# Optimization experiments

Measured on AMD Instinct MI355X. Metric: run time of the kernel, lower is better.

The kernel has to match this reference:

```python
import jax, jax.numpy as jnp
import numpy as np

B, N, D_IN = 256, 64, 128   # batch, n_agents, input_dim
H0, H1, H2 = 256, 256, 64   # rnn_hidden_dim[0], [1], [2]


def setup_inputs() -> dict:
    key = jax.random.key(0)
    ks = jax.random.split(key, 14)
    s = 0.05
    return {
        "obs": jax.random.normal(ks[0], (B, N, D_IN), dtype=jnp.float32),
        "W_enc": jax.random.normal(ks[1], (H0, D_IN), dtype=jnp.float32) * s,
        "b_enc": jax.random.normal(ks[2], (H0,), dtype=jnp.float32) * s,
        "W_obs": jax.random.normal(ks[3], (H0, H0), dtype=jnp.float32) * s,
        "b_obs": jax.random.normal(ks[4], (H0,), dtype=jnp.float32) * s,
        "W_ih": jax.random.normal(ks[5], (3 * H0, H0), dtype=jnp.float32) * s,
        "b_ih": jax.random.normal(ks[6], (3 * H0,), dtype=jnp.float32) * s,
        "W_hh": jax.random.normal(ks[7], (3 * H0, H0), dtype=jnp.float32) * s,
        "b_hh": jax.random.normal(ks[8], (3 * H0,), dtype=jnp.float32) * s,
        "W_val": jax.random.normal(ks[9], (H1, H0), dtype=jnp.float32) * s,
        "b_val": jax.random.normal(ks[10], (H1,), dtype=jnp.float32) * s,
        "W_dec": jax.random.normal(ks[11], (H2, H1), dtype=jnp.float32) * s,
        "b_dec": jax.random.normal(ks[12], (H2,), dtype=jnp.float32) * s,
    }


def reference(obs, W_enc, b_enc, W_obs, b_obs, W_ih, b_ih, W_hh, b_hh,
              W_val, b_val, W_dec, b_dec):
    # encoding + f_obs  -> h: [B, N, H0]
    x = jax.nn.relu(jnp.einsum("bnd,hd->bnh", obs, W_enc) + b_enc)
    h = jnp.einsum("bnh,gh->bng", x, W_obs) + b_obs

    # comm: mean over other agents. Original masks self and divides by N
    # (mean over dim of size N with self zeroed) => (sum_all - self) / N.
    c = (jnp.sum(h, axis=1, keepdims=True) - h) / N  # [B, N, H0]

    # GRUCell(input=c, hidden=h), PyTorch gate ordering r, z, n
    gi = jnp.einsum("bnh,gh->bng", c, W_ih) + b_ih   # [B, N, 3*H0]
    gh = jnp.einsum("bnh,gh->bng", h, W_hh) + b_hh
    gi_r, gi_z, gi_n = jnp.split(gi, 3, axis=-1)
    gh_r, gh_z, gh_n = jnp.split(gh, 3, axis=-1)
    r = jax.nn.sigmoid(gi_r + gh_r)
    z = jax.nn.sigmoid(gi_z + gh_z)
    n = jnp.tanh(gi_n + r * gh_n)
    h = (1.0 - z) * n + z * h  # [B, N, H0]

    # value head + decoding; seq_len=1 squeezed -> [B, N, H2]
    v = jnp.einsum("bnh,vh->bnv", h, W_val) + b_val
    out = jnp.einsum("bnv,ov->bno", v, W_dec) + b_dec
    return out
```

## Files before the change

kernel.cpp:

```cpp
#include <hip/hip_runtime.h>
#include <hip/hip_bf16.h>
#include <math.h>


typedef __bf16  bf16x8 __attribute__((ext_vector_type(8)));
typedef float   f32x4  __attribute__((ext_vector_type(4)));

#define DIN 128
#define H0  256
#define SW  264
#define SWO 136
#define LOG2E 1.44269504088896f

#define O_WENC 0
#define O_WOBS 32768
#define O_WIH  98304
#define O_WHH  294912
#define O_WVAL 491520
#define O_WDEC 557056
#define W_TOT  573440

__device__ __forceinline__ f32x4 mfma16(bf16x8 a, bf16x8 b, f32x4 c) {
    return __builtin_amdgcn_mfma_f32_16x16x32_bf16(a, b, c, 0, 0, 0);
}
__device__ __forceinline__ float bf2f(__hip_bfloat16 x) { return __bfloat162float(x); }
__device__ __forceinline__ __hip_bfloat16 f2bf(float x) { return __float2bfloat16(x); }

__device__ __forceinline__ float fsigmoid(float x) {
    float e = __builtin_amdgcn_exp2f(-LOG2E * x);
    return __builtin_amdgcn_rcpf(1.0f + e);
}
__device__ __forceinline__ float ftanh(float x) {
    float e = __builtin_amdgcn_exp2f(2.0f * LOG2E * x);
    return 1.0f - 2.0f * __builtin_amdgcn_rcpf(1.0f + e);
}

__device__ __forceinline__ bf16x8 w8(const __hip_bfloat16* p, int idx) {
    return *(const bf16x8*)(p + idx);
}

__device__ __forceinline__ int tadr(int r, int k) { return r * SW + k; }
__device__ __forceinline__ int oadr(int r, int k) { return r * SWO + k; }

__global__ __launch_bounds__(256) void prep_kernel(
    const float* __restrict__ W_enc, const float* __restrict__ W_obs,
    const float* __restrict__ W_ih,  const float* __restrict__ W_hh,
    const float* __restrict__ W_val, const float* __restrict__ W_dec,
    __hip_bfloat16* __restrict__ ws)
{
    const int i = (blockIdx.x * 256 + threadIdx.x) * 8;
    if (i >= W_TOT) return;
    const float* src; int off;
    if      (i < O_WOBS) { src = W_enc; off = O_WENC; }
    else if (i < O_WIH)  { src = W_obs; off = O_WOBS; }
    else if (i < O_WHH)  { src = W_ih;  off = O_WIH;  }
    else if (i < O_WVAL) { src = W_hh;  off = O_WHH;  }
    else if (i < O_WDEC) { src = W_val; off = O_WVAL; }
    else                 { src = W_dec; off = O_WDEC; }
    const float* f = src + (i - off);
    f32x4 a = *(const f32x4*)f;
    f32x4 b = *(const f32x4*)(f + 4);
    bf16x8 v;
    #pragma unroll
    for (int j = 0; j < 4; j++) { v[j] = (__bf16)a[j]; v[j + 4] = (__bf16)b[j]; }
    *(bf16x8*)(ws + i) = v;
}

__global__ __launch_bounds__(512, 2) void commnet_mfma(
    const __hip_bfloat16* __restrict__ ws,
    const float* __restrict__ b_enc, const float* __restrict__ b_obs,
    const float* __restrict__ b_ih,  const float* __restrict__ b_hh,
    const float* __restrict__ b_val, const float* __restrict__ b_dec,
    const float* __restrict__ obs,   float* __restrict__ out)
{
    __shared__ __align__(16) __hip_bfloat16 T0[64 * SW];
    __shared__ __align__(16) __hip_bfloat16 T1[64 * SW];

    const __hip_bfloat16* W_enc = ws + O_WENC;
    const __hip_bfloat16* W_obs = ws + O_WOBS;
    const __hip_bfloat16* W_ih  = ws + O_WIH;
    const __hip_bfloat16* W_hh  = ws + O_WHH;
    const __hip_bfloat16* W_val = ws + O_WVAL;
    const __hip_bfloat16* W_dec = ws + O_WDEC;

    const int tid  = threadIdx.x;
    const int wave = tid >> 6;
    const int lane = tid & 63;
    const int quad = lane >> 4;
    const int lc   = lane & 15;
    const int row0 = blockIdx.x * 64;
    const int ko16 = quad * 8;

    for (int i = tid; i < 64 * DIN / 8; i += 512) {
        const int r = i >> 4;
        const int c = (i & 15) << 3;
        const float* src = obs + (row0 + r) * DIN + c;
        f32x4 a = *(const f32x4*)src;
        f32x4 b = *(const f32x4*)(src + 4);
        bf16x8 v;
        #pragma unroll
        for (int j = 0; j < 4; j++) { v[j] = (__bf16)a[j]; v[j + 4] = (__bf16)b[j]; }
        *(bf16x8*)&T1[oadr(r, c)] = v;
    }
    __syncthreads();

    #pragma unroll
    for (int cp = 0; cp < 2; cp++) {
        const int n = (wave + 8 * cp) * 16 + lc;
        const float bias = b_enc[n];
        f32x4 acc[4] = {};
        #pragma unroll
        for (int k0 = 0; k0 < DIN; k0 += 32) {
            const int kk = k0 + ko16;
            bf16x8 b = w8(W_enc, n * DIN + kk);
            #pragma unroll
            for (int rt = 0; rt < 4; rt++) {
                bf16x8 a = *(const bf16x8*)&T1[oadr(rt * 16 + lc, kk)];
                acc[rt] = mfma16(a, b, acc[rt]);
            }
        }
        #pragma unroll
        for (int rt = 0; rt < 4; rt++)
            #pragma unroll
            for (int i = 0; i < 4; i++) {
                const int row = rt * 16 + quad * 4 + i;
                T0[tadr(row, n)] = f2bf(fmaxf(acc[rt][i] + bias, 0.0f));
            }
    }
    __syncthreads();

    #pragma unroll
    for (int cp = 0; cp < 2; cp++) {
        const int n = (wave + 8 * cp) * 16 + lc;
        const float bias = b_obs[n];
        f32x4 acc[4] = {};
        #pragma unroll 2
        for (int k0 = 0; k0 < H0; k0 += 32) {
            const int kk = k0 + ko16;
            bf16x8 b = w8(W_obs, n * H0 + kk);
            #pragma unroll
            for (int rt = 0; rt < 4; rt++) {
                bf16x8 a = *(const bf16x8*)&T0[tadr(rt * 16 + lc, kk)];
                acc[rt] = mfma16(a, b, acc[rt]);
            }
        }
        #pragma unroll
        for (int rt = 0; rt < 4; rt++)
            #pragma unroll
            for (int i = 0; i < 4; i++) {
                const int row = rt * 16 + quad * 4 + i;
                T1[tadr(row, n)] = f2bf(acc[rt][i] + bias);
            }
    }
    __syncthreads();

    #pragma unroll
    for (int cp = 0; cp < 2; cp++) {
        const int n = (wave + 8 * cp) * 16 + lc;
        const float bir = b_ih[n], biz = b_ih[n + 256], bin = b_ih[n + 512];
        const float bhr = b_hh[n], bhz = b_hh[n + 256], bhn = b_hh[n + 512];
        f32x4 gir[4] = {}, giz[4] = {}, gin[4] = {};
        f32x4 ghr[4] = {}, ghz[4] = {}, ghn[4] = {};
        #pragma unroll 2
        for (int k0 = 0; k0 < H0; k0 += 32) {
            const int kk = k0 + ko16;
            bf16x8 bir8 = w8(W_ih, (n      ) * H0 + kk);
            bf16x8 biz8 = w8(W_ih, (n + 256) * H0 + kk);
            bf16x8 bin8 = w8(W_ih, (n + 512) * H0 + kk);
            bf16x8 bhr8 = w8(W_hh, (n      ) * H0 + kk);
            bf16x8 bhz8 = w8(W_hh, (n + 256) * H0 + kk);
            bf16x8 bhn8 = w8(W_hh, (n + 512) * H0 + kk);
            #pragma unroll
            for (int rt = 0; rt < 4; rt++) {
                bf16x8 aH = *(const bf16x8*)&T1[tadr(rt * 16 + lc, kk)];
                gir[rt] = mfma16(aH, bir8, gir[rt]);
                giz[rt] = mfma16(aH, biz8, giz[rt]);
                gin[rt] = mfma16(aH, bin8, gin[rt]);
                ghr[rt] = mfma16(aH, bhr8, ghr[rt]);
                ghz[rt] = mfma16(aH, bhz8, ghz[rt]);
                ghn[rt] = mfma16(aH, bhn8, ghn[rt]);
            }
        }
        float Sr = 0.0f, Sz = 0.0f, Sn = 0.0f;
        #pragma unroll
        for (int rt = 0; rt < 4; rt++)
            #pragma unroll
            for (int i = 0; i < 4; i++) {
                Sr += gir[rt][i]; Sz += giz[rt][i]; Sn += gin[rt][i];
            }
        Sr += __shfl_xor(Sr, 16); Sr += __shfl_xor(Sr, 32);
        Sz += __shfl_xor(Sz, 16); Sz += __shfl_xor(Sz, 32);
        Sn += __shfl_xor(Sn, 16); Sn += __shfl_xor(Sn, 32);

        #pragma unroll
        for (int rt = 0; rt < 4; rt++)
            #pragma unroll
            for (int i = 0; i < 4; i++) {
                const int row = rt * 16 + quad * 4 + i;
                const float gi_r = (Sr - gir[rt][i]) * (1.0f / 64.0f) + bir;
                const float gi_z = (Sz - giz[rt][i]) * (1.0f / 64.0f) + biz;
                const float gi_n = (Sn - gin[rt][i]) * (1.0f / 64.0f) + bin;
                const float r  = fsigmoid(gi_r + ghr[rt][i] + bhr);
                const float z  = fsigmoid(gi_z + ghz[rt][i] + bhz);
                const float nn = ftanh(gi_n + r * (ghn[rt][i] + bhn));
                const float h  = bf2f(T1[tadr(row, n)]);
                T0[tadr(row, n)] = f2bf((1.0f - z) * nn + z * h);
            }
    }
    __syncthreads();

    #pragma unroll
    for (int cp = 0; cp < 2; cp++) {
        const int n = (wave + 8 * cp) * 16 + lc;
        const float bias = b_val[n];
        f32x4 acc[4] = {};
        #pragma unroll 2
        for (int k0 = 0; k0 < H0; k0 += 32) {
            const int kk = k0 + ko16;
            bf16x8 b = w8(W_val, n * H0 + kk);
            #pragma unroll
            for (int rt = 0; rt < 4; rt++) {
                bf16x8 a = *(const bf16x8*)&T0[tadr(rt * 16 + lc, kk)];
                acc[rt] = mfma16(a, b, acc[rt]);
            }
        }
        #pragma unroll
        for (int rt = 0; rt < 4; rt++)
            #pragma unroll
            for (int i = 0; i < 4; i++) {
                const int row = rt * 16 + quad * 4 + i;
                T1[tadr(row, n)] = f2bf(acc[rt][i] + bias);
            }
    }
    __syncthreads();

    {
        const int ct  = wave & 3;
        const int rtb = (wave >> 2) * 2;
        const int n   = ct * 16 + lc;
        const float bias = b_dec[n];
        f32x4 acc[2] = {};
        #pragma unroll 2
        for (int k0 = 0; k0 < H0; k0 += 32) {
            const int kk = k0 + ko16;
            bf16x8 b = w8(W_dec, n * H0 + kk);
            #pragma unroll
            for (int j = 0; j < 2; j++) {
                bf16x8 a = *(const bf16x8*)&T1[tadr((rtb + j) * 16 + lc, kk)];
                acc[j] = mfma16(a, b, acc[j]);
            }
        }
        #pragma unroll
        for (int j = 0; j < 2; j++)
            #pragma unroll
            for (int i = 0; i < 4; i++) {
                const int row = (rtb + j) * 16 + quad * 4 + i;
                out[(row0 + row) * 64 + n] = acc[j][i] + bias;
            }
    }
}

extern "C" void kernel_launch(void* const* d_in, const int* in_sizes, int n_in,
                              void* d_out, int out_size, void* d_ws, size_t ws_size,
                              hipStream_t stream) {
    (void)in_sizes; (void)n_in; (void)out_size; (void)ws_size;
    const float* obs   = (const float*)d_in[0];
    const float* W_enc = (const float*)d_in[1];  const float* b_enc = (const float*)d_in[2];
    const float* W_obs = (const float*)d_in[3];  const float* b_obs = (const float*)d_in[4];
    const float* W_ih  = (const float*)d_in[5];  const float* b_ih  = (const float*)d_in[6];
    const float* W_hh  = (const float*)d_in[7];  const float* b_hh  = (const float*)d_in[8];
    const float* W_val = (const float*)d_in[9];  const float* b_val = (const float*)d_in[10];
    const float* W_dec = (const float*)d_in[11]; const float* b_dec = (const float*)d_in[12];
    float* out = (float*)d_out;
    __hip_bfloat16* ws = (__hip_bfloat16*)d_ws;

    prep_kernel<<<280, 256, 0, stream>>>(W_enc, W_obs, W_ih, W_hh, W_val, W_dec, ws);
    commnet_mfma<<<256, 512, 0, stream>>>(
        ws, b_enc, b_obs, b_ih, b_hh, b_val, b_dec, obs, out);
}
```

Measured before the change: 122.6 us.

## Split fused kernel into encoder and GRU kernels with 32-row blocks

Splits the single fused kernel into two launches: an encoder kernel that writes h to workspace along with per-block column sums, and a GRU/value/decode kernel that reads them back. Each block now handles 32 rows, so there are 512 blocks instead of 256, which gives more blocks per CU. The communication term is computed as an MFMA of the column sum against W_ih, so the per-row input-gate matmuls are no longer scaled. Costs include an extra launch, a global round trip of h, and the gi matmul still running on h; a fallback to the fused kernel is kept for when the workspace is too small.

```diff
diff --git a/kernel.cpp b/kernel.cpp
--- a/kernel.cpp
+++ b/kernel.cpp
@@ -19,6 +19,9 @@
 #define O_WVAL 491520
 #define O_WDEC 557056
 #define W_TOT  573440
+#define O_H    573440
+#define B_PARTS 9535488
+#define WS_NEED (9535488 + 524288)
 
 __device__ __forceinline__ f32x4 mfma16(bf16x8 a, bf16x8 b, f32x4 c) {
     return __builtin_amdgcn_mfma_f32_16x16x32_bf16(a, b, c, 0, 0, 0);
@@ -34,13 +37,9 @@
     float e = __builtin_amdgcn_exp2f(2.0f * LOG2E * x);
     return 1.0f - 2.0f * __builtin_amdgcn_rcpf(1.0f + e);
 }
-
 __device__ __forceinline__ bf16x8 w8(const __hip_bfloat16* p, int idx) {
     return *(const bf16x8*)(p + idx);
 }
-
-__device__ __forceinline__ int tadr(int r, int k) { return r * SW + k; }
-__device__ __forceinline__ int oadr(int r, int k) { return r * SWO + k; }
 
 __global__ __launch_bounds__(256) void prep_kernel(
     const float* __restrict__ W_enc, const float* __restrict__ W_obs,
@@ -66,7 +65,229 @@
     *(bf16x8*)(ws + i) = v;
 }
 
-__global__ __launch_bounds__(512, 2) void commnet_mfma(
+__global__ __launch_bounds__(512, 2) void k_enc(
+    const __hip_bfloat16* __restrict__ ws,
+    const float* __restrict__ b_enc, const float* __restrict__ b_obs,
+    const float* __restrict__ obs,
+    __hip_bfloat16* __restrict__ Hws, float* __restrict__ parts)
+{
+    __shared__ __align__(16) __hip_bfloat16 OB[32 * SWO];
+    __shared__ __align__(16) __hip_bfloat16 X1[32 * SW];
+    __shared__ __align__(16) __hip_bfloat16 HT[32 * SW];
+
+    const __hip_bfloat16* W_enc = ws + O_WENC;
+    const __hip_bfloat16* W_obs = ws + O_WOBS;
+
+    const int tid  = threadIdx.x;
+    const int wave = tid >> 6;
+    const int lane = tid & 63;
+    const int quad = lane >> 4;
+    const int lc   = lane & 15;
+    const int ko16 = quad * 8;
+    const int R0   = blockIdx.x * 32;
+
+    {
+        const int r = tid >> 4;
+        const int c = (tid & 15) << 3;
+        const float* src = obs + (R0 + r) * DIN + c;
+        f32x4 a = *(const f32x4*)src;
+        f32x4 b = *(const f32x4*)(src + 4);
+        bf16x8 v;
+        #pragma unroll
+        for (int j = 0; j < 4; j++) { v[j] = (__bf16)a[j]; v[j + 4] = (__bf16)b[j]; }
+        *(bf16x8*)&OB[r * SWO + c] = v;
+    }
+    __syncthreads();
+
+    #pragma unroll
+    for (int cp = 0; cp < 2; cp++) {
+        const int n = (wave + 8 * cp) * 16 + lc;
+        const float bias = b_enc[n];
+        f32x4 acc[2] = {};
+        #pragma unroll
+        for (int k0 = 0; k0 < DIN; k0 += 32) {
+            const int kk = k0 + ko16;
+            bf16x8 b = w8(W_enc, n * DIN + kk);
+            #pragma unroll
+            for (int rt = 0; rt < 2; rt++) {
+                bf16x8 a = *(const bf16x8*)&OB[(rt * 16 + lc) * SWO + kk];
+                acc[rt] = mfma16(a, b, acc[rt]);
+            }
+        }
+        #pragma unroll
+        for (int rt = 0; rt < 2; rt++)
+            #pragma unroll
+            for (int i = 0; i < 4; i++)
+                X1[(rt * 16 + quad * 4 + i) * SW + n] = f2bf(fmaxf(acc[rt][i] + bias, 0.0f));
+    }
+    __syncthreads();
+
+    #pragma unroll
+    for (int cp = 0; cp < 2; cp++) {
+        const int n = (wave + 8 * cp) * 16 + lc;
+        const float bias = b_obs[n];
+        f32x4 acc[2] = {};
+        #pragma unroll 2
+        for (int k0 = 0; k0 < H0; k0 += 32) {
+            const int kk = k0 + ko16;
+            bf16x8 b = w8(W_obs, n * H0 + kk);
+            #pragma unroll
+            for (int rt = 0; rt < 2; rt++) {
+                bf16x8 a = *(const bf16x8*)&X1[(rt * 16 + lc) * SW + kk];
+                acc[rt] = mfma16(a, b, acc[rt]);
+            }
+        }
+        float colp = 0.0f;
+        #pragma unroll
+        for (int rt = 0; rt < 2; rt++)
+            #pragma unroll
+            for (int i = 0; i < 4; i++) {
+                const float v = acc[rt][i] + bias;
+                HT[(rt * 16 + quad * 4 + i) * SW + n] = f2bf(v);
+                colp += v;
+            }
+        colp += __shfl_xor(colp, 16);
+        colp += __shfl_xor(colp, 32);
+        if (quad == 0) parts[blockIdx.x * 256 + n] = colp;
+    }
+    __syncthreads();
+
+    {
+        const int r = tid >> 4;
+        const int c = (tid << 4) & 255;
+        *(bf16x8*)&Hws[(R0 + r) * 256 + c]     = *(const bf16x8*)&HT[r * SW + c];
+        *(bf16x8*)&Hws[(R0 + r) * 256 + c + 8] = *(const bf16x8*)&HT[r * SW + c + 8];
+    }
+}
+
+__global__ __launch_bounds__(512, 2) void k_gru(
+    const __hip_bfloat16* __restrict__ ws,
+    const float* __restrict__ b_ih,  const float* __restrict__ b_hh,
+    const float* __restrict__ b_val, const float* __restrict__ b_dec,
+    const __hip_bfloat16* __restrict__ Hws, const float* __restrict__ parts,
+    float* __restrict__ out)
+{
+    __shared__ __align__(16) __hip_bfloat16 HT[32 * SW];
+    __shared__ __align__(16) __hip_bfloat16 HP[32 * SW];
+    __shared__ __align__(16) __hip_bfloat16 CS[256];
+
+    const __hip_bfloat16* W_ih  = ws + O_WIH;
+    const __hip_bfloat16* W_hh  = ws + O_WHH;
+    const __hip_bfloat16* W_val = ws + O_WVAL;
+    const __hip_bfloat16* W_dec = ws + O_WDEC;
+
+    const int tid  = threadIdx.x;
+    const int wave = tid >> 6;
+    const int lane = tid & 63;
+    const int quad = lane >> 4;
+    const int lc   = lane & 15;
+    const int ko16 = quad * 8;
+    const int R0   = blockIdx.x * 32;
+    const int pb   = blockIdx.x & ~1;
+
+    {
+        const int r = tid >> 4;
+        const int c = (tid << 4) & 255;
+        *(bf16x8*)&HT[r * SW + c]     = *(const bf16x8*)&Hws[(R0 + r) * 256 + c];
+        *(bf16x8*)&HT[r * SW + c + 8] = *(const bf16x8*)&Hws[(R0 + r) * 256 + c + 8];
+        if (tid < 256)
+            CS[tid] = f2bf(parts[pb * 256 + tid] + parts[(pb + 1) * 256 + tid]);
+    }
+    __syncthreads();
+
+    #pragma unroll
+    for (int cp = 0; cp < 2; cp++) {
+        const int n = (wave + 8 * cp) * 16 + lc;
+        const float bir = b_ih[n], biz = b_ih[n + 256], bin = b_ih[n + 512];
+        const float bhr = b_hh[n], bhz = b_hh[n + 256], bhn = b_hh[n + 512];
+        f32x4 gir[2] = {}, giz[2] = {}, gin[2] = {};
+        f32x4 ghr[2] = {}, ghz[2] = {}, ghn[2] = {};
+        f32x4 sr = {}, sz = {}, sn = {};
+        #pragma unroll 2
+        for (int k0 = 0; k0 < H0; k0 += 32) {
+            const int kk = k0 + ko16;
+            bf16x8 csA = *(const bf16x8*)&CS[kk];
+            bf16x8 bir8 = w8(W_ih, (n      ) * H0 + kk);
+            bf16x8 biz8 = w8(W_ih, (n + 256) * H0 + kk);
+            bf16x8 bin8 = w8(W_ih, (n + 512) * H0 + kk);
+            bf16x8 bhr8 = w8(W_hh, (n      ) * H0 + kk);
+            bf16x8 bhz8 = w8(W_hh, (n + 256) * H0 + kk);
+            bf16x8 bhn8 = w8(W_hh, (n + 512) * H0 + kk);
+            sr = mfma16(csA, bir8, sr);
+            sz = mfma16(csA, biz8, sz);
+            sn = mfma16(csA, bin8, sn);
+            #pragma unroll
+            for (int rt = 0; rt < 2; rt++) {
+                bf16x8 aH = *(const bf16x8*)&HT[(rt * 16 + lc) * SW + kk];
+                gir[rt] = mfma16(aH, bir8, gir[rt]);
+                giz[rt] = mfma16(aH, biz8, giz[rt]);
+                gin[rt] = mfma16(aH, bin8, gin[rt]);
+                ghr[rt] = mfma16(aH, bhr8, ghr[rt]);
+                ghz[rt] = mfma16(aH, bhz8, ghz[rt]);
+                ghn[rt] = mfma16(aH, bhn8, ghn[rt]);
+            }
+        }
+        const float s_r = sr[0], s_z = sz[0], s_n = sn[0];
+        #pragma unroll
+        for (int rt = 0; rt < 2; rt++)
+            #pragma unroll
+            for (int i = 0; i < 4; i++) {
+                const int row = rt * 16 + quad * 4 + i;
+                const float gi_r = (s_r - gir[rt][i]) * (1.0f / 64.0f) + bir;
+                const float gi_z = (s_z - giz[rt][i]) * (1.0f / 64.0f) + biz;
+                const float gi_n = (s_n - gin[rt][i]) * (1.0f / 64.0f) + bin;
+                const float r  = fsigmoid(gi_r + ghr[rt][i] + bhr);
+                const float z  = fsigmoid(gi_z + ghz[rt][i] + bhz);
+                const float nn = ftanh(gi_n + r * (ghn[rt][i] + bhn));
+                const float h  = bf2f(HT[row * SW + n]);
+                HP[row * SW + n] = f2bf((1.0f - z) * nn + z * h);
+            }
+    }
+    __syncthreads();
+
+    #pragma unroll
+    for (int cp = 0; cp < 2; cp++) {
+        const int n = (wave + 8 * cp) * 16 + lc;
+        const float bias = b_val[n];
+        f32x4 acc[2] = {};
+        #pragma unroll 2
+        for (int k0 = 0; k0 < H0; k0 += 32) {
+            const int kk = k0 + ko16;
+            bf16x8 b = w8(W_val, n * H0 + kk);
+            #pragma unroll
+            for (int rt = 0; rt < 2; rt++) {
+                bf16x8 a = *(const bf16x8*)&HP[(rt * 16 + lc) * SW + kk];
+                acc[rt] = mfma16(a, b, acc[rt]);
+            }
+        }
+        #pragma unroll
+        for (int rt = 0; rt < 2; rt++)
+            #pragma unroll
+            for (int i = 0; i < 4; i++)
+                HT[(rt * 16 + quad * 4 + i) * SW + n] = f2bf(acc[rt][i] + bias);
+    }
+    __syncthreads();
+
+    {
+        const int ct = wave & 3;
+        const int rt = wave >> 2;
+        const int n  = ct * 16 + lc;
+        const float bias = b_dec[n];
+        f32x4 acc = {};
+        #pragma unroll 2
+        for (int k0 = 0; k0 < H0; k0 += 32) {
+            const int kk = k0 + ko16;
+            bf16x8 b = w8(W_dec, n * H0 + kk);
+            bf16x8 a = *(const bf16x8*)&HT[(rt * 16 + lc) * SW + kk];
+            acc = mfma16(a, b, acc);
+        }
+        #pragma unroll
+        for (int i = 0; i < 4; i++)
+            out[(R0 + rt * 16 + quad * 4 + i) * 64 + n] = acc[i] + bias;
+    }
+}
+
+__global__ __launch_bounds__(512, 2) void commnet_fused(
     const __hip_bfloat16* __restrict__ ws,
     const float* __restrict__ b_enc, const float* __restrict__ b_obs,
     const float* __restrict__ b_ih,  const float* __restrict__ b_hh,
@@ -100,7 +321,7 @@
         bf16x8 v;
         #pragma unroll
         for (int j = 0; j < 4; j++) { v[j] = (__bf16)a[j]; v[j + 4] = (__bf16)b[j]; }
-        *(bf16x8*)&T1[oadr(r, c)] = v;
+        *(bf16x8*)&T1[r * SWO + c] = v;
     }
     __syncthreads();
 
@@ -115,17 +336,15 @@
             bf16x8 b = w8(W_enc, n * DIN + kk);
             #pragma unroll
             for (int rt = 0; rt < 4; rt++) {
-                bf16x8 a = *(const bf16x8*)&T1[oadr(rt * 16 + lc, kk)];
+                bf16x8 a = *(const bf16x8*)&T1[(rt * 16 + lc) * SWO + kk];
                 acc[rt] = mfma16(a, b, acc[rt]);
             }
         }
         #pragma unroll
         for (int rt = 0; rt < 4; rt++)
             #pragma unroll
-            for (int i = 0; i < 4; i++) {
-                const int row = rt * 16 + quad * 4 + i;
-                T0[tadr(row, n)] = f2bf(fmaxf(acc[rt][i] + bias, 0.0f));
-            }
+            for (int i = 0; i < 4; i++)
+                T0[(rt * 16 + quad * 4 + i) * SW + n] = f2bf(fmaxf(acc[rt][i] + bias, 0.0f));
     }
     __syncthreads();
 
@@ -140,17 +359,15 @@
             bf16x8 b = w8(W_obs, n * H0 + kk);
             #pragma unroll
             for (int rt = 0; rt < 4; rt++) {
-                bf16x8 a = *(const bf16x8*)&T0[tadr(rt * 16 + lc, kk)];
+                bf16x8 a = *(const bf16x8*)&T0[(rt * 16 + lc) * SW + kk];
                 acc[rt] = mfma16(a, b, acc[rt]);
             }
         }
         #pragma unroll
         for (int rt = 0; rt < 4; rt++)
             #pragma unroll
-            for (int i = 0; i < 4; i++) {
-                const int row = rt * 16 + quad * 4 + i;
-                T1[tadr(row, n)] = f2bf(acc[rt][i] + bias);
-            }
+            for (int i = 0; i < 4; i++)
+                T1[(rt * 16 + quad * 4 + i) * SW + n] = f2bf(acc[rt][i] + bias);
     }
     __syncthreads();
 
@@ -172,7 +389,7 @@
             bf16x8 bhn8 = w8(W_hh, (n + 512) * H0 + kk);
             #pragma unroll
             for (int rt = 0; rt < 4; rt++) {
-                bf16x8 aH = *(const bf16x8*)&T1[tadr(rt * 16 + lc, kk)];
+                bf16x8 aH = *(const bf16x8*)&T1[(rt * 16 + lc) * SW + kk];
                 gir[rt] = mfma16(aH, bir8, gir[rt]);
                 giz[rt] = mfma16(aH, biz8, giz[rt]);
                 gin[rt] = mfma16(aH, bin8, gin[rt]);
@@ -191,7 +408,6 @@
         Sr += __shfl_xor(Sr, 16); Sr += __shfl_xor(Sr, 32);
         Sz += __shfl_xor(Sz, 16); Sz += __shfl_xor(Sz, 32);
         Sn += __shfl_xor(Sn, 16); Sn += __shfl_xor(Sn, 32);
-
         #pragma unroll
         for (int rt = 0; rt < 4; rt++)
             #pragma unroll
@@ -203,8 +419,8 @@
                 const float r  = fsigmoid(gi_r + ghr[rt][i] + bhr);
                 const float z  = fsigmoid(gi_z + ghz[rt][i] + bhz);
                 const float nn = ftanh(gi_n + r * (ghn[rt][i] + bhn));
-                const float h  = bf2f(T1[tadr(row, n)]);
-                T0[tadr(row, n)] = f2bf((1.0f - z) * nn + z * h);
+                const float h  = bf2f(T1[row * SW + n]);
+                T0[row * SW + n] = f2bf((1.0f - z) * nn + z * h);
             }
     }
     __syncthreads();
@@ -220,17 +436,15 @@
             bf16x8 b = w8(W_val, n * H0 + kk);
             #pragma unroll
             for (int rt = 0; rt < 4; rt++) {
-                bf16x8 a = *(const bf16x8*)&T0[tadr(rt * 16 + lc, kk)];
+                bf16x8 a = *(const bf16x8*)&T0[(rt * 16 + lc) * SW + kk];
                 acc[rt] = mfma16(a, b, acc[rt]);
             }
         }
         #pragma unroll
         for (int rt = 0; rt < 4; rt++)
             #pragma unroll
-            for (int i = 0; i < 4; i++) {
-                const int row = rt * 16 + quad * 4 + i;
-                T1[tadr(row, n)] = f2bf(acc[rt][i] + bias);
-            }
+            for (int i = 0; i < 4; i++)
+                T1[(rt * 16 + quad * 4 + i) * SW + n] = f2bf(acc[rt][i] + bias);
     }
     __syncthreads();
 
@@ -246,7 +460,7 @@
             bf16x8 b = w8(W_dec, n * H0 + kk);
             #pragma unroll
             for (int j = 0; j < 2; j++) {
-                bf16x8 a = *(const bf16x8*)&T1[tadr((rtb + j) * 16 + lc, kk)];
+                bf16x8 a = *(const bf16x8*)&T1[((rtb + j) * 16 + lc) * SW + kk];
                 acc[j] = mfma16(a, b, acc[j]);
             }
         }
@@ -263,7 +477,7 @@
 extern "C" void kernel_launch(void* const* d_in, const int* in_sizes, int n_in,
                               void* d_out, int out_size, void* d_ws, size_t ws_size,
                               hipStream_t stream) {
-    (void)in_sizes; (void)n_in; (void)out_size; (void)ws_size;
+    (void)in_sizes; (void)n_in; (void)out_size;
     const float* obs   = (const float*)d_in[0];
     const float* W_enc = (const float*)d_in[1];  const float* b_enc = (const float*)d_in[2];
     const float* W_obs = (const float*)d_in[3];  const float* b_obs = (const float*)d_in[4];
@@ -275,6 +489,14 @@
     __hip_bfloat16* ws = (__hip_bfloat16*)d_ws;
 
     prep_kernel<<<280, 256, 0, stream>>>(W_enc, W_obs, W_ih, W_hh, W_val, W_dec, ws);
-    commnet_mfma<<<256, 512, 0, stream>>>(
-        ws, b_enc, b_obs, b_ih, b_hh, b_val, b_dec, obs, out);
-}
+
+    if (ws_size >= (size_t)WS_NEED) {
+        __hip_bfloat16* Hws  = ws + O_H;
+        float* parts = (float*)((char*)d_ws + B_PARTS);
+        k_enc<<<512, 512, 0, stream>>>(ws, b_enc, b_obs, obs, Hws, parts);
+        k_gru<<<512, 512, 0, stream>>>(ws, b_ih, b_hh, b_val, b_dec, Hws, parts, out);
+    } else {
+        commnet_fused<<<256, 512, 0, stream>>>(
+            ws, b_enc, b_obs, b_ih, b_hh, b_val, b_dec, obs, out);
+    }
+}
```

Measured after the change: 160.5 us. +30.9%, slower.

## Stage weights through double-buffered swizzled LDS with cooperative prefetch

Applied to the files above, without the earlier changes.

Weight tiles are now loaded cooperatively by the whole block into a double-buffered LDS buffer. The next 64-wide k-slice is prefetched into registers while MFMAs consume the current one, instead of each lane reading weights straight from global memory. Activation buffers switch from padded strides to an XOR-swizzled layout to avoid bank conflicts. GRU gates are processed one gate at a time across k-blocks. LDS use rises to 128 KB per block, which can cut occupancy below two blocks per CU, and a barrier is added per k-slice.

```diff
diff --git a/kernel.cpp b/kernel.cpp
--- a/kernel.cpp
+++ b/kernel.cpp
@@ -8,8 +8,6 @@
 
 #define DIN 128
 #define H0  256
-#define SW  264
-#define SWO 136
 #define LOG2E 1.44269504088896f
 
 #define O_WENC 0
@@ -25,7 +23,6 @@
 }
 __device__ __forceinline__ float bf2f(__hip_bfloat16 x) { return __bfloat162float(x); }
 __device__ __forceinline__ __hip_bfloat16 f2bf(float x) { return __float2bfloat16(x); }
-
 __device__ __forceinline__ float fsigmoid(float x) {
     float e = __builtin_amdgcn_exp2f(-LOG2E * x);
     return __builtin_amdgcn_rcpf(1.0f + e);
@@ -34,13 +31,60 @@
     float e = __builtin_amdgcn_exp2f(2.0f * LOG2E * x);
     return 1.0f - 2.0f * __builtin_amdgcn_rcpf(1.0f + e);
 }
-
 __device__ __forceinline__ bf16x8 w8(const __hip_bfloat16* p, int idx) {
     return *(const bf16x8*)(p + idx);
 }
 
-__device__ __forceinline__ int tadr(int r, int k) { return r * SW + k; }
-__device__ __forceinline__ int oadr(int r, int k) { return r * SWO + k; }
+__device__ __forceinline__ int tadr(int r, int k) {
+    return (r << 8) + ((((k >> 3) ^ r) & 31) << 3) + (k & 7);
+}
+__device__ __forceinline__ int oadr(int r, int k) {
+    return (r << 7) + ((((k >> 3) ^ r) & 15) << 3) + (k & 7);
+}
+
+struct St4 { bf16x8 v[4]; };
+
+__device__ __forceinline__ St4 ld_sq(const __hip_bfloat16* src, int K, int kb, int tid) {
+    St4 s;
+    #pragma unroll
+    for (int j = 0; j < 4; j++) {
+        const int u = tid + j * 512, n = u >> 3, c = u & 7;
+        s.v[j] = w8(src, n * K + kb * 64 + c * 8);
+    }
+    return s;
+}
+__device__ __forceinline__ void st_sq(__hip_bfloat16* dst, const St4& s, int tid) {
+    #pragma unroll
+    for (int j = 0; j < 4; j++) {
+        const int u = tid + j * 512, n = u >> 3, c = u & 7;
+        *(bf16x8*)&dst[n * 64 + ((c ^ (n & 7)) << 3)] = s.v[j];
+    }
+}
+__device__ __forceinline__ bf16x8 rd_sq(const __hip_bfloat16* wb, int n, int kw) {
+    return *(const bf16x8*)&wb[n * 64 + ((((kw >> 3) ^ (n & 7)) & 7) << 3)];
+}
+
+__device__ __forceinline__ St4 ld_gr(const __hip_bfloat16* Wih, const __hip_bfloat16* Whh,
+                                     int p, int cp, int kb, int tid) {
+    St4 s;
+    #pragma unroll
+    for (int j = 0; j < 4; j++) {
+        const int u = tid + j * 512, g2 = u >> 10, rem = u & 1023, nl = rem >> 3, c = rem & 7;
+        const __hip_bfloat16* m = g2 ? Whh : Wih;
+        s.v[j] = w8(m, (p * 256 + cp * 128 + nl) * 256 + kb * 64 + c * 8);
+    }
+    return s;
+}
+__device__ __forceinline__ void st_gr(__hip_bfloat16* dst, const St4& s, int tid) {
+    #pragma unroll
+    for (int j = 0; j < 4; j++) {
+        const int u = tid + j * 512, g2 = u >> 10, rem = u & 1023, nl = rem >> 3, c = rem & 7;
+        *(bf16x8*)&dst[g2 * 8192 + nl * 64 + ((c ^ (nl & 7)) << 3)] = s.v[j];
+    }
+}
+__device__ __forceinline__ bf16x8 rd_gr(const __hip_bfloat16* wb, int g2, int nl, int kw) {
+    return *(const bf16x8*)&wb[g2 * 8192 + nl * 64 + ((((kw >> 3) ^ (nl & 7)) & 7) << 3)];
+}
 
 __global__ __launch_bounds__(256) void prep_kernel(
     const float* __restrict__ W_enc, const float* __restrict__ W_obs,
@@ -66,15 +110,16 @@
     *(bf16x8*)(ws + i) = v;
 }
 
-__global__ __launch_bounds__(512, 2) void commnet_mfma(
+__global__ __launch_bounds__(512, 2) void commnet_v6(
     const __hip_bfloat16* __restrict__ ws,
     const float* __restrict__ b_enc, const float* __restrict__ b_obs,
     const float* __restrict__ b_ih,  const float* __restrict__ b_hh,
     const float* __restrict__ b_val, const float* __restrict__ b_dec,
     const float* __restrict__ obs,   float* __restrict__ out)
 {
-    __shared__ __align__(16) __hip_bfloat16 T0[64 * SW];
-    __shared__ __align__(16) __hip_bfloat16 T1[64 * SW];
+    __shared__ __align__(16) __hip_bfloat16 T0[16384];
+    __shared__ __align__(16) __hip_bfloat16 T1[16384];
+    __shared__ __align__(16) __hip_bfloat16 WBb[32768];
 
     const __hip_bfloat16* W_enc = ws + O_WENC;
     const __hip_bfloat16* W_obs = ws + O_WOBS;
@@ -90,160 +135,223 @@
     const int lc   = lane & 15;
     const int row0 = blockIdx.x * 64;
     const int ko16 = quad * 8;
-
-    for (int i = tid; i < 64 * DIN / 8; i += 512) {
-        const int r = i >> 4;
-        const int c = (i & 15) << 3;
-        const float* src = obs + (row0 + r) * DIN + c;
-        f32x4 a = *(const f32x4*)src;
-        f32x4 b = *(const f32x4*)(src + 4);
-        bf16x8 v;
-        #pragma unroll
-        for (int j = 0; j < 4; j++) { v[j] = (__bf16)a[j]; v[j + 4] = (__bf16)b[j]; }
-        *(bf16x8*)&T1[oadr(r, c)] = v;
-    }
-    __syncthreads();
-
-    #pragma unroll
-    for (int cp = 0; cp < 2; cp++) {
-        const int n = (wave + 8 * cp) * 16 + lc;
-        const float bias = b_enc[n];
-        f32x4 acc[4] = {};
-        #pragma unroll
-        for (int k0 = 0; k0 < DIN; k0 += 32) {
-            const int kk = k0 + ko16;
-            bf16x8 b = w8(W_enc, n * DIN + kk);
-            #pragma unroll
-            for (int rt = 0; rt < 4; rt++) {
-                bf16x8 a = *(const bf16x8*)&T1[oadr(rt * 16 + lc, kk)];
-                acc[rt] = mfma16(a, b, acc[rt]);
-            }
-        }
-        #pragma unroll
-        for (int rt = 0; rt < 4; rt++)
-            #pragma unroll
-            for (int i = 0; i < 4; i++) {
-                const int row = rt * 16 + quad * 4 + i;
-                T0[tadr(row, n)] = f2bf(fmaxf(acc[rt][i] + bias, 0.0f));
-            }
-    }
-    __syncthreads();
-
-    #pragma unroll
-    for (int cp = 0; cp < 2; cp++) {
-        const int n = (wave + 8 * cp) * 16 + lc;
-        const float bias = b_obs[n];
-        f32x4 acc[4] = {};
-        #pragma unroll 2
+    const int n0   = wave * 16 + lc;
+    const int n1   = n0 + 128;
+
+    {
+        #pragma unroll
+        for (int j = 0; j < 2; j++) {
+            const int u = tid + j * 512;
+            const int r = u >> 4, c = (u & 15) << 3;
+            const float* src = obs + (row0 + r) * DIN + c;
+            f32x4 a = *(const f32x4*)src;
+            f32x4 b = *(const f32x4*)(src + 4);
+            bf16x8 v;
+            #pragma unroll
+            for (int q = 0; q < 4; q++) { v[q] = (__bf16)a[q]; v[q + 4] = (__bf16)b[q]; }
+            *(bf16x8*)&T1[oadr(r, c)] = v;
+        }
+        St4 s0 = ld_sq(W_enc, DIN, 0, tid);
+        st_sq(WBb, s0, tid);
+    }
+    __syncthreads();
+
+    {
+        f32x4 acc[2][4] = {};
+        #pragma unroll
+        for (int kb = 0; kb < 2; kb++) {
+            St4 nx = (kb == 0) ? ld_sq(W_enc, DIN, 1, tid) : ld_sq(W_obs, H0, 0, tid);
+            const __hip_bfloat16* wb = WBb + (kb & 1) * 16384;
+            #pragma unroll
+            for (int ki = 0; ki < 2; ki++) {
+                const int kt = kb * 64 + ki * 32 + ko16;
+                const int kw = ki * 32 + ko16;
+                bf16x8 a[4];
+                #pragma unroll
+                for (int rt = 0; rt < 4; rt++) a[rt] = *(const bf16x8*)&T1[oadr(rt * 16 + lc, kt)];
+                bf16x8 b0 = rd_sq(wb, n0, kw);
+                bf16x8 b1 = rd_sq(wb, n1, kw);
+                #pragma unroll
+                for (int rt = 0; rt < 4; rt++) {
+                    acc[0][rt] = mfma16(a[rt], b0, acc[0][rt]);
+                    acc[1][rt] = mfma16(a[rt], b1, acc[1][rt]);
+                }
+            }
+            st_sq(WBb + ((kb + 1) & 1) * 16384, nx, tid);
+            __syncthreads();
+        }
+        #pragma unroll
+        for (int cp = 0; cp < 2; cp++) {
+            const int n = cp ? n1 : n0;
+            const float bias = b_enc[n];
+            #pragma unroll
+            for (int rt = 0; rt < 4; rt++)
+                #pragma unroll
+                for (int i = 0; i < 4; i++)
+                    T0[tadr(rt * 16 + quad * 4 + i, n)] = f2bf(fmaxf(acc[cp][rt][i] + bias, 0.0f));
+        }
+    }
+    __syncthreads();
+
+    {
+        f32x4 acc[2][4] = {};
+        #pragma unroll
+        for (int kb = 0; kb < 4; kb++) {
+            St4 nx;
+            if (kb < 3) nx = ld_sq(W_obs, H0, kb + 1, tid);
+            else        nx = ld_gr(W_ih, W_hh, 0, 0, 0, tid);
+            const __hip_bfloat16* wb = WBb + (kb & 1) * 16384;
+            #pragma unroll
+            for (int ki = 0; ki < 2; ki++) {
+                const int kt = kb * 64 + ki * 32 + ko16;
+                const int kw = ki * 32 + ko16;
+                bf16x8 a[4];
+                #pragma unroll
+                for (int rt = 0; rt < 4; rt++) a[rt] = *(const bf16x8*)&T0[tadr(rt * 16 + lc, kt)];
+                bf16x8 b0 = rd_sq(wb, n0, kw);
+                bf16x8 b1 = rd_sq(wb, n1, kw);
+                #pragma unroll
+                for (int rt = 0; rt < 4; rt++) {
+                    acc[0][rt] = mfma16(a[rt], b0, acc[0][rt]);
+                    acc[1][rt] = mfma16(a[rt], b1, acc[1][rt]);
+                }
+            }
+            if (kb < 3) st_sq(WBb + ((kb + 1) & 1) * 16384, nx, tid);
+            else        st_gr(WBb + ((kb + 1) & 1) * 16384, nx, tid);
+            __syncthreads();
+        }
+        #pragma unroll
+        for (int cp = 0; cp < 2; cp++) {
+            const int n = cp ? n1 : n0;
+            const float bias = b_obs[n];
+            #pragma unroll
+            for (int rt = 0; rt < 4; rt++)
+                #pragma unroll
+                for (int i = 0; i < 4; i++)
+                    T1[tadr(rt * 16 + quad * 4 + i, n)] = f2bf(acc[cp][rt][i] + bias);
+        }
+    }
+    __syncthreads();
+
+    {
+        int g = 0;
+        #pragma unroll
+        for (int cp = 0; cp < 2; cp++) {
+            f32x4 acc[6][4] = {};
+            #pragma unroll
+            for (int kb = 0; kb < 4; kb++) {
+                #pragma unroll
+                for (int p = 0; p < 3; p++) {
+                    int pn = p + 1, kbn = kb, cpn = cp;
+                    if (pn == 3) { pn = 0; kbn++; if (kbn == 4) { kbn = 0; cpn++; } }
+                    St4 nx;
+                    if (cpn < 2) nx = ld_gr(W_ih, W_hh, pn, cpn, kbn, tid);
+                    else         nx = ld_sq(W_val, H0, 0, tid);
+                    const __hip_bfloat16* wb = WBb + (g & 1) * 16384;
+                    #pragma unroll
+                    for (int ki = 0; ki < 2; ki++) {
+                        const int kt = kb * 64 + ki * 32 + ko16;
+                        const int kw = ki * 32 + ko16;
+                        bf16x8 a[4];
+                        #pragma unroll
+                        for (int rt = 0; rt < 4; rt++)
+                            a[rt] = *(const bf16x8*)&T1[tadr(rt * 16 + lc, kt)];
+                        bf16x8 bi = rd_gr(wb, 0, n0, kw);
+                        bf16x8 bh = rd_gr(wb, 1, n0, kw);
+                        #pragma unroll
+                        for (int rt = 0; rt < 4; rt++) {
+                            acc[p][rt]     = mfma16(a[rt], bi, acc[p][rt]);
+                            acc[3 + p][rt] = mfma16(a[rt], bh, acc[3 + p][rt]);
+                        }
+                    }
+                    if (cpn < 2) st_gr(WBb + ((g + 1) & 1) * 16384, nx, tid);
+                    else         st_sq(WBb + ((g + 1) & 1) * 16384, nx, tid);
+                    __syncthreads();
+                    g++;
+                }
+            }
+            {
+                const int n = cp ? n1 : n0;
+                const float bir = b_ih[n], biz = b_ih[n + 256], bin = b_ih[n + 512];
+                const float bhr = b_hh[n], bhz = b_hh[n + 256], bhn = b_hh[n + 512];
+                float Sr = 0.0f, Sz = 0.0f, Sn = 0.0f;
+                #pragma unroll
+                for (int rt = 0; rt < 4; rt++)
+                    #pragma unroll
+                    for (int i = 0; i < 4; i++) {
+                        Sr += acc[0][rt][i]; Sz += acc[1][rt][i]; Sn += acc[2][rt][i];
+                    }
+                Sr += __shfl_xor(Sr, 16); Sr += __shfl_xor(Sr, 32);
+                Sz += __shfl_xor(Sz, 16); Sz += __shfl_xor(Sz, 32);
+                Sn += __shfl_xor(Sn, 16); Sn += __shfl_xor(Sn, 32);
+                #pragma unroll
+                for (int rt = 0; rt < 4; rt++)
+                    #pragma unroll
+                    for (int i = 0; i < 4; i++) {
+                        const int row = rt * 16 + quad * 4 + i;
+                        const float gi_r = (Sr - acc[0][rt][i]) * (1.0f / 64.0f) + bir;
+                        const float gi_z = (Sz - acc[1][rt][i]) * (1.0f / 64.0f) + biz;
+                        const float gi_n = (Sn - acc[2][rt][i]) * (1.0f / 64.0f) + bin;
+                        const float r  = fsigmoid(gi_r + acc[3][rt][i] + bhr);
+                        const float z  = fsigmoid(gi_z + acc[4][rt][i] + bhz);
+                        const float nn = ftanh(gi_n + r * (acc[5][rt][i] + bhn));
+                        const float h  = bf2f(T1[tadr(row, n)]);
+                        T0[tadr(row, n)] = f2bf((1.0f - z) * nn + z * h);
+                    }
+            }
+        }
+    }
+    __syncthreads();
+
+    {
+        f32x4 acc[2][4] = {};
+        #pragma unroll
+        for (int kb = 0; kb < 4; kb++) {
+            St4 nx;
+            const bool hn = kb < 3;
+            if (hn) nx = ld_sq(W_val, H0, kb + 1, tid);
+            const __hip_bfloat16* wb = WBb + (kb & 1) * 16384;
+            #pragma unroll
+            for (int ki = 0; ki < 2; ki++) {
+                const int kt = kb * 64 + ki * 32 + ko16;
+                const int kw = ki * 32 + ko16;
+                bf16x8 a[4];
+                #pragma unroll
+                for (int rt = 0; rt < 4; rt++) a[rt] = *(const bf16x8*)&T0[tadr(rt * 16 + lc, kt)];
+                bf16x8 b0 = rd_sq(wb, n0, kw);
+                bf16x8 b1 = rd_sq(wb, n1, kw);
+                #pragma unroll
+                for (int rt = 0; rt < 4; rt++) {
+                    acc[0][rt] = mfma16(a[rt], b0, acc[0][rt]);
+                    acc[1][rt] = mfma16(a[rt], b1, acc[1][rt]);
+                }
+            }
+            if (hn) st_sq(WBb + ((kb + 1) & 1) * 16384, nx, tid);
+            __syncthreads();
+        }
+        #pragma unroll
+        for (int cp = 0; cp < 2; cp++) {
+            const int n = cp ? n1 : n0;
+            const float bias = b_val[n];
+            #pragma unroll
+            for (int rt = 0; rt < 4; rt++)
+                #pragma unroll
+                for (int i = 0; i < 4; i++)
+                    T1[tadr(rt * 16 + quad * 4 + i, n)] = f2bf(acc[cp][rt][i] + bias);
+        }
+    }
+    __syncthreads();
+
+    {
+        const int ct  = wave & 3;
+        const int rtb = (wave >> 2) * 2;
+        const int nd  = ct * 16 + lc;
+        const float bias = b_dec[nd];
+        f32x4 acc[2] = {};
+        #pragma unroll
         for (int k0 = 0; k0 < H0; k0 += 32) {
             const int kk = k0 + ko16;
-            bf16x8 b = w8(W_obs, n * H0 + kk);
-            #pragma unroll
-            for (int rt = 0; rt < 4; rt++) {
-                bf16x8 a = *(const bf16x8*)&T0[tadr(rt * 16 + lc, kk)];
-                acc[rt] = mfma16(a, b, acc[rt]);
-            }
-        }
-        #pragma unroll
-        for (int rt = 0; rt < 4; rt++)
-            #pragma unroll
-            for (int i = 0; i < 4; i++) {
-                const int row = rt * 16 + quad * 4 + i;
-                T1[tadr(row, n)] = f2bf(acc[rt][i] + bias);
-            }
-    }
-    __syncthreads();
-
-    #pragma unroll
-    for (int cp = 0; cp < 2; cp++) {
-        const int n = (wave + 8 * cp) * 16 + lc;
-        const float bir = b_ih[n], biz = b_ih[n + 256], bin = b_ih[n + 512];
-        const float bhr = b_hh[n], bhz = b_hh[n + 256], bhn = b_hh[n + 512];
-        f32x4 gir[4] = {}, giz[4] = {}, gin[4] = {};
-        f32x4 ghr[4] = {}, ghz[4] = {}, ghn[4] = {};
-        #pragma unroll 2
-        for (int k0 = 0; k0 < H0; k0 += 32) {
-            const int kk = k0 + ko16;
-            bf16x8 bir8 = w8(W_ih, (n      ) * H0 + kk);
-            bf16x8 biz8 = w8(W_ih, (n + 256) * H0 + kk);
-            bf16x8 bin8 = w8(W_ih, (n + 512) * H0 + kk);
-            bf16x8 bhr8 = w8(W_hh, (n      ) * H0 + kk);
-            bf16x8 bhz8 = w8(W_hh, (n + 256) * H0 + kk);
-            bf16x8 bhn8 = w8(W_hh, (n + 512) * H0 + kk);
-            #pragma unroll
-            for (int rt = 0; rt < 4; rt++) {
-                bf16x8 aH = *(const bf16x8*)&T1[tadr(rt * 16 + lc, kk)];
-                gir[rt] = mfma16(aH, bir8, gir[rt]);
-                giz[rt] = mfma16(aH, biz8, giz[rt]);
-                gin[rt] = mfma16(aH, bin8, gin[rt]);
-                ghr[rt] = mfma16(aH, bhr8, ghr[rt]);
-                ghz[rt] = mfma16(aH, bhz8, ghz[rt]);
-                ghn[rt] = mfma16(aH, bhn8, ghn[rt]);
-            }
-        }
-        float Sr = 0.0f, Sz = 0.0f, Sn = 0.0f;
-        #pragma unroll
-        for (int rt = 0; rt < 4; rt++)
-            #pragma unroll
-            for (int i = 0; i < 4; i++) {
-                Sr += gir[rt][i]; Sz += giz[rt][i]; Sn += gin[rt][i];
-            }
-        Sr += __shfl_xor(Sr, 16); Sr += __shfl_xor(Sr, 32);
-        Sz += __shfl_xor(Sz, 16); Sz += __shfl_xor(Sz, 32);
-        Sn += __shfl_xor(Sn, 16); Sn += __shfl_xor(Sn, 32);
-
-        #pragma unroll
-        for (int rt = 0; rt < 4; rt++)
-            #pragma unroll
-            for (int i = 0; i < 4; i++) {
-                const int row = rt * 16 + quad * 4 + i;
-                const float gi_r = (Sr - gir[rt][i]) * (1.0f / 64.0f) + bir;
-                const float gi_z = (Sz - giz[rt][i]) * (1.0f / 64.0f) + biz;
-                const float gi_n = (Sn - gin[rt][i]) * (1.0f / 64.0f) + bin;
-                const float r  = fsigmoid(gi_r + ghr[rt][i] + bhr);
-                const float z  = fsigmoid(gi_z + ghz[rt][i] + bhz);
-                const float nn = ftanh(gi_n + r * (ghn[rt][i] + bhn));
-                const float h  = bf2f(T1[tadr(row, n)]);
-                T0[tadr(row, n)] = f2bf((1.0f - z) * nn + z * h);
-            }
-    }
-    __syncthreads();
-
-    #pragma unroll
-    for (int cp = 0; cp < 2; cp++) {
-        const int n = (wave + 8 * cp) * 16 + lc;
-        const float bias = b_val[n];
-        f32x4 acc[4] = {};
-        #pragma unroll 2
-        for (int k0 = 0; k0 < H0; k0 += 32) {
-            const int kk = k0 + ko16;
-            bf16x8 b = w8(W_val, n * H0 + kk);
-            #pragma unroll
-            for (int rt = 0; rt < 4; rt++) {
-                bf16x8 a = *(const bf16x8*)&T0[tadr(rt * 16 + lc, kk)];
-                acc[rt] = mfma16(a, b, acc[rt]);
-            }
-        }
-        #pragma unroll
-        for (int rt = 0; rt < 4; rt++)
-            #pragma unroll
-            for (int i = 0; i < 4; i++) {
-                const int row = rt * 16 + quad * 4 + i;
-                T1[tadr(row, n)] = f2bf(acc[rt][i] + bias);
-            }
-    }
-    __syncthreads();
-
-    {
-        const int ct  = wave & 3;
-        const int rtb = (wave >> 2) * 2;
-        const int n   = ct * 16 + lc;
-        const float bias = b_dec[n];
-        f32x4 acc[2] = {};
-        #pragma unroll 2
-        for (int k0 = 0; k0 < H0; k0 += 32) {
-            const int kk = k0 + ko16;
-            bf16x8 b = w8(W_dec, n * H0 + kk);
+            bf16x8 b = w8(W_dec, nd * H0 + kk);
             #pragma unroll
             for (int j = 0; j < 2; j++) {
                 bf16x8 a = *(const bf16x8*)&T1[tadr((rtb + j) * 16 + lc, kk)];
@@ -255,7 +363,7 @@
             #pragma unroll
             for (int i = 0; i < 4; i++) {
                 const int row = (rtb + j) * 16 + quad * 4 + i;
-                out[(row0 + row) * 64 + n] = acc[j][i] + bias;
+                out[(row0 + row) * 64 + nd] = acc[j][i] + bias;
             }
     }
 }
@@ -275,6 +383,6 @@
     __hip_bfloat16* ws = (__hip_bfloat16*)d_ws;
 
     prep_kernel<<<280, 256, 0, stream>>>(W_enc, W_obs, W_ih, W_hh, W_val, W_dec, ws);
-    commnet_mfma<<<256, 512, 0, stream>>>(
+    commnet_v6<<<256, 512, 0, stream>>>(
         ws, b_enc, b_obs, b_ih, b_hh, b_val, b_dec, obs, out);
 }
```

Measured after the change: 154.4 us. 25.9% more time.
